# Performance work log

Measured on AMD Instinct MI355X. Metric: run time of the kernel, lower is better.

The kernel has to match this reference:

```python
import jax, jax.numpy as jnp
import numpy as np

T, B, C = 1024, 16, 1024
H, K, PAD_L = 16, 7, 3  # num_heads, kernel_size, padding_l
OUT = 1024


def setup_inputs() -> dict:
    key = jax.random.key(0)
    ks = jax.random.split(key, 8)
    s_in = 1.0 / np.sqrt(C)
    return {
        "x": jax.random.normal(ks[0], (T, B, C), dtype=jnp.float32),
        "W1": jax.random.normal(ks[1], (C, C), dtype=jnp.float32) * s_in,
        "b1": jnp.zeros((C,), dtype=jnp.float32),
        "Wq": jax.random.normal(ks[2], (C, H * K), dtype=jnp.float32) * s_in,
        "bq": jnp.zeros((H * K,), dtype=jnp.float32),
        "conv_bias": jax.random.normal(ks[3], (C,), dtype=jnp.float32) * 0.02,
        "W2": jax.random.normal(ks[4], (C, OUT), dtype=jnp.float32) * s_in,
        "b2": jnp.zeros((OUT,), dtype=jnp.float32),
    }


def reference(x, W1, b1, Wq, bq, conv_bias, W2, b2):
    # linear1 (glu=False -> no activation)
    h = x @ W1 + b1                       # [T, B, C]
    Tn, Bn, Cn = h.shape
    R = Cn // H                           # channels per head
    # dynamic filter prediction from query (= h), softmax over K taps
    w = (h @ Wq + bq).reshape(Tn, Bn, H, K)
    w = jax.nn.softmax(w, axis=-1)        # [T, B, H, K]
    # unfold1d: pad PAD_L left, K-1-PAD_L right along time, gather K-windows
    hp = jnp.pad(h, ((PAD_L, K - 1 - PAD_L), (0, 0), (0, 0)))
    win = jnp.stack([hp[k:k + Tn] for k in range(K)], axis=-1)  # [T, B, C, K]
    win = win.reshape(Tn, Bn, H, R, K)
    out = jnp.einsum('tbhrk,tbhk->tbhr', win, w).reshape(Tn, Bn, Cn)
    out = out + conv_bias                 # [T, B, C]
    return out @ W2 + b2                  # [T, B, OUT]
```

## Files before the change

kernel.cpp:

```cpp
#include <hip/hip_runtime.h>
#include <math.h>

#define T_DIM 1024
#define B_DIM 16
#define C_DIM 1024
#define H_DIM 16
#define K_TAPS 7
#define PAD_LEFT 3
#define OUT_DIM 1024
#define M_DIM (T_DIM * B_DIM)
#define HK 112
#define HKP 128
#define KD 1024
#define NT32 (KD / 32)

typedef __attribute__((ext_vector_type(8))) short bf16x8;
typedef __attribute__((ext_vector_type(4))) float f32x4;

__device__ __forceinline__ ushort f2bf(float f) {
    union { float f; unsigned u; } v; v.f = f;
    unsigned u = v.u;
    u += 0x7fffu + ((u >> 16) & 1u);
    return (ushort)(u >> 16);
}
__device__ __forceinline__ float bf2f(ushort h) {
    union { unsigned u; float f; } v; v.u = ((unsigned)h) << 16;
    return v.f;
}

__global__ __launch_bounds__(256) void cvt_bf16x8(const float* __restrict__ in,
                                                  ushort* __restrict__ out,
                                                  int n8) {
    int i = blockIdx.x * blockDim.x + threadIdx.x;
    if (i >= n8) return;
    const float4* p = (const float4*)in;
    float4 a = p[2 * i], b = p[2 * i + 1];
    uint4 o;
    o.x = (unsigned)f2bf(a.x) | ((unsigned)f2bf(a.y) << 16);
    o.y = (unsigned)f2bf(a.z) | ((unsigned)f2bf(a.w) << 16);
    o.z = (unsigned)f2bf(b.x) | ((unsigned)f2bf(b.y) << 16);
    o.w = (unsigned)f2bf(b.z) | ((unsigned)f2bf(b.w) << 16);
    ((uint4*)out)[i] = o;
}

__global__ void transpose_cvt(const float* __restrict__ W,
                              ushort* __restrict__ Wt,
                              int Kd, int N, int Npad) {
    __shared__ float tile[32][33];
    int n0 = blockIdx.x * 32, k0 = blockIdx.y * 32;
    int tx = threadIdx.x, ty = threadIdx.y;
#pragma unroll
    for (int j = 0; j < 4; ++j) {
        int k = k0 + ty * 4 + j;
        int n = n0 + tx;
        tile[ty * 4 + j][tx] = (n < N) ? W[(size_t)k * N + n] : 0.f;
    }
    __syncthreads();
#pragma unroll
    for (int j = 0; j < 4; ++j) {
        int n = n0 + ty * 4 + j;
        if (n < Npad)
            Wt[(size_t)n * Kd + k0 + tx] = f2bf(tile[tx][ty * 4 + j]);
    }
}

template <bool OUT_BF16>
__global__ __launch_bounds__(256, 2) void gemm_k32(
    const ushort* __restrict__ A, const ushort* __restrict__ Bt,
    const float* __restrict__ bias, void* __restrict__ Cp, int ldc) {
    __shared__ ushort Ab[2][256 * 32];
    __shared__ ushort Bb[2][128 * 32];

    const int tid  = threadIdx.x;
    const int lane = tid & 63;
    const int wid  = tid >> 6;
    const int wr = wid >> 1;
    const int wc = wid & 1;
    const int fr = lane & 15;
    const int fq = lane >> 4;

    const int orig = blockIdx.x;
    const int nid  = (orig & 7) * 64 + (orig >> 3);
    const int bm = (nid >> 3) * 256;
    const int bn = (nid & 7) * 128;

    const int rA   = tid >> 2;
    const int slA  = (tid & 3) * 8;
    const size_t srcA0 = (size_t)(bm + rA) * KD + slA;
    const size_t srcB0 = (size_t)(bn + rA) * KD + slA;

    const int aBase0 = (wr * 128 + fr) * 32 + fq * 8;
    const int bBase0 = (wc * 64 + fr) * 32 + fq * 8;

    f32x4 acc[8][4];
#pragma unroll
    for (int m = 0; m < 8; ++m)
#pragma unroll
        for (int n = 0; n < 4; ++n) acc[m][n] = (f32x4){0.f, 0.f, 0.f, 0.f};

    auto stage = [&](int buf, int t) {
        const ushort* Ap = A + srcA0 + t * 32;
        const ushort* Bp = Bt + srcB0 + t * 32;
#pragma unroll
        for (int i = 0; i < 4; ++i)
            __builtin_amdgcn_global_load_lds(
                (const __attribute__((address_space(1))) void*)(Ap + (size_t)i * 64 * KD),
                (__attribute__((address_space(3))) void*)(&Ab[buf][(i * 256 + wid * 64) * 8]),
                16, 0, 0);
#pragma unroll
        for (int i = 0; i < 2; ++i)
            __builtin_amdgcn_global_load_lds(
                (const __attribute__((address_space(1))) void*)(Bp + (size_t)i * 64 * KD),
                (__attribute__((address_space(3))) void*)(&Bb[buf][(i * 256 + wid * 64) * 8]),
                16, 0, 0);
    };

    stage(0, 0);
    stage(1, 1);
    asm volatile("s_waitcnt vmcnt(6)" ::: "memory");
    __builtin_amdgcn_sched_barrier(0);
    __builtin_amdgcn_s_barrier();

#pragma unroll 1
    for (int t = 0; t < NT32; ++t) {
        const int cur = t & 1;
        const ushort* Ac = &Ab[cur][0];
        const ushort* Bc = &Bb[cur][0];

        bf16x8 a[8], b[4];
#pragma unroll
        for (int n = 0; n < 4; ++n)
            b[n] = *(const bf16x8*)(Bc + bBase0 + n * 512);
#pragma unroll
        for (int m = 0; m < 8; ++m)
            a[m] = *(const bf16x8*)(Ac + aBase0 + m * 512);

        asm volatile("s_waitcnt lgkmcnt(0)" ::: "memory");
        __builtin_amdgcn_sched_barrier(0);
        __builtin_amdgcn_s_barrier();

        if (t < NT32 - 2) stage(cur, t + 2);

        __builtin_amdgcn_s_setprio(1);
#pragma unroll
        for (int m = 0; m < 8; ++m)
#pragma unroll
            for (int n = 0; n < 4; ++n)
                acc[m][n] = __builtin_amdgcn_mfma_f32_16x16x32_bf16(
                    a[m], b[n], acc[m][n], 0, 0, 0);
        __builtin_amdgcn_s_setprio(0);

        if (t < NT32 - 2) {
            asm volatile("s_waitcnt vmcnt(6)" ::: "memory");
        } else if (t == NT32 - 2) {
            asm volatile("s_waitcnt vmcnt(0)" ::: "memory");
        }
        __builtin_amdgcn_sched_barrier(0);
        if (t < NT32 - 1) __builtin_amdgcn_s_barrier();
    }

#pragma unroll
    for (int n = 0; n < 4; ++n) {
        int col = bn + wc * 64 + n * 16 + fr;
        float bv = bias[col];
#pragma unroll
        for (int m = 0; m < 8; ++m) {
#pragma unroll
            for (int r = 0; r < 4; ++r) {
                int row = bm + wr * 128 + m * 16 + fq * 4 + r;
                float v = acc[m][n][r] + bv;
                if (OUT_BF16)
                    ((ushort*)Cp)[(size_t)row * ldc + col] = f2bf(v);
                else
                    ((float*)Cp)[(size_t)row * ldc + col] = v;
            }
        }
    }
}

template <bool OUT_BF16, bool NGUARD>
__global__ __launch_bounds__(256) void gemm_mfma(const ushort* __restrict__ A,
                                                 const ushort* __restrict__ Bt,
                                                 const float* __restrict__ bias,
                                                 void* __restrict__ Cp,
                                                 int Kd, int N, int ldc) {
    __shared__ ushort Als[128 * 32];
    __shared__ ushort Bls[128 * 32];
    const int tid  = threadIdx.x;
    const int lane = tid & 63;
    const int wid  = tid >> 6;
    const int wr = wid >> 1, wc = wid & 1;
    const int bm = blockIdx.y * 128, bn = blockIdx.x * 128;
    const int fq = lane >> 4, fr = lane & 15;

    f32x4 acc[4][4];
#pragma unroll
    for (int m = 0; m < 4; ++m)
#pragma unroll
        for (int n = 0; n < 4; ++n) acc[m][n] = (f32x4){0.f, 0.f, 0.f, 0.f};

    const int c0 = wid * 128 + lane;
    const int c1 = c0 + 64;
    const int r0 = c0 >> 2, o0 = (c0 & 3) * 8;
    const int r1 = c1 >> 2, o1 = (c1 & 3) * 8;

    for (int k0 = 0; k0 < Kd; k0 += 32) {
        __builtin_amdgcn_global_load_lds(
            (const __attribute__((address_space(1))) void*)&A[(size_t)(bm + r0) * Kd + k0 + o0],
            (__attribute__((address_space(3))) void*)&Als[(wid * 2 + 0) * 512], 16, 0, 0);
        __builtin_amdgcn_global_load_lds(
            (const __attribute__((address_space(1))) void*)&A[(size_t)(bm + r1) * Kd + k0 + o1],
            (__attribute__((address_space(3))) void*)&Als[(wid * 2 + 1) * 512], 16, 0, 0);
        __builtin_amdgcn_global_load_lds(
            (const __attribute__((address_space(1))) void*)&Bt[(size_t)(bn + r0) * Kd + k0 + o0],
            (__attribute__((address_space(3))) void*)&Bls[(wid * 2 + 0) * 512], 16, 0, 0);
        __builtin_amdgcn_global_load_lds(
            (const __attribute__((address_space(1))) void*)&Bt[(size_t)(bn + r1) * Kd + k0 + o1],
            (__attribute__((address_space(3))) void*)&Bls[(wid * 2 + 1) * 512], 16, 0, 0);
        __syncthreads();

        bf16x8 af[4], bfr[4];
#pragma unroll
        for (int m = 0; m < 4; ++m)
            af[m] = *(const bf16x8*)&Als[(wr * 64 + m * 16 + fr) * 32 + fq * 8];
#pragma unroll
        for (int n = 0; n < 4; ++n)
            bfr[n] = *(const bf16x8*)&Bls[(wc * 64 + n * 16 + fr) * 32 + fq * 8];
#pragma unroll
        for (int m = 0; m < 4; ++m)
#pragma unroll
            for (int n = 0; n < 4; ++n)
                acc[m][n] = __builtin_amdgcn_mfma_f32_16x16x32_bf16(
                    af[m], bfr[n], acc[m][n], 0, 0, 0);
        __syncthreads();
    }

#pragma unroll
    for (int m = 0; m < 4; ++m) {
#pragma unroll
        for (int n = 0; n < 4; ++n) {
            int col = bn + wc * 64 + n * 16 + fr;
            if (NGUARD && col >= N) continue;
            float bv = bias[col];
#pragma unroll
            for (int r = 0; r < 4; ++r) {
                int row = bm + wr * 64 + m * 16 + fq * 4 + r;
                float v = acc[m][n][r] + bv;
                if (OUT_BF16)
                    ((ushort*)Cp)[(size_t)row * ldc + col] = f2bf(v);
                else
                    ((float*)Cp)[(size_t)row * ldc + col] = v;
            }
        }
    }
}

__global__ __launch_bounds__(256) void dynconv_bf16(const ushort* __restrict__ h,
                                                    const float* __restrict__ q,
                                                    const float* __restrict__ cbias,
                                                    ushort* __restrict__ out) {
    const int m = blockIdx.x;
    const int t = m >> 4;
    const int b = m & 15;

    __shared__ float wsm[HK];
    if (threadIdx.x < HK)
        wsm[threadIdx.x] = q[(size_t)m * HK + threadIdx.x];
    __syncthreads();
    if (threadIdx.x < H_DIM) {
        float* p = &wsm[threadIdx.x * K_TAPS];
        float mx = p[0];
#pragma unroll
        for (int k = 1; k < K_TAPS; ++k) mx = fmaxf(mx, p[k]);
        float e[K_TAPS], s = 0.f;
#pragma unroll
        for (int k = 0; k < K_TAPS; ++k) { e[k] = __expf(p[k] - mx); s += e[k]; }
        float inv = 1.f / s;
#pragma unroll
        for (int k = 0; k < K_TAPS; ++k) p[k] = e[k] * inv;
    }
    __syncthreads();

    const int c = threadIdx.x * 4;
    const int hh = c >> 6;

    float4 bias = *(const float4*)&cbias[c];
    float a0 = bias.x, a1 = bias.y, a2 = bias.z, a3 = bias.w;

#pragma unroll
    for (int k = 0; k < K_TAPS; ++k) {
        int tt = t + k - PAD_LEFT;
        if (tt < 0 || tt >= T_DIM) continue;
        ushort4 hv = *(const ushort4*)&h[((size_t)tt * B_DIM + b) * C_DIM + c];
        float wk = wsm[hh * K_TAPS + k];
        a0 = fmaf(bf2f(hv.x), wk, a0);
        a1 = fmaf(bf2f(hv.y), wk, a1);
        a2 = fmaf(bf2f(hv.z), wk, a2);
        a3 = fmaf(bf2f(hv.w), wk, a3);
    }
    ushort4 o;
    o.x = f2bf(a0); o.y = f2bf(a1); o.z = f2bf(a2); o.w = f2bf(a3);
    *(ushort4*)&out[(size_t)m * C_DIM + c] = o;
}

extern "C" void kernel_launch(void* const* d_in, const int* in_sizes, int n_in,
                              void* d_out, int out_size, void* d_ws,
                              size_t ws_size, hipStream_t stream) {
    const float* x     = (const float*)d_in[0];
    const float* W1    = (const float*)d_in[1];
    const float* b1    = (const float*)d_in[2];
    const float* Wq    = (const float*)d_in[3];
    const float* bq    = (const float*)d_in[4];
    const float* cbias = (const float*)d_in[5];
    const float* W2    = (const float*)d_in[6];
    const float* b2    = (const float*)d_in[7];
    float* out = (float*)d_out;

    ushort* xb    = (ushort*)d_ws;
    ushort* hb    = xb    + (size_t)M_DIM * C_DIM;
    ushort* convb = hb    + (size_t)M_DIM * C_DIM;
    ushort* W1t   = convb + (size_t)M_DIM * C_DIM;
    ushort* W2t   = W1t   + (size_t)C_DIM * C_DIM;
    ushort* Wqt   = W2t   + (size_t)C_DIM * OUT_DIM;
    float*  q     = (float*)(Wqt + (size_t)HKP * C_DIM);

    cvt_bf16x8<<<dim3(M_DIM * C_DIM / 8 / 256), dim3(256), 0, stream>>>(
        x, xb, M_DIM * C_DIM / 8);
    transpose_cvt<<<dim3(C_DIM / 32, C_DIM / 32), dim3(32, 8), 0, stream>>>(
        W1, W1t, C_DIM, C_DIM, C_DIM);
    transpose_cvt<<<dim3(HKP / 32, C_DIM / 32), dim3(32, 8), 0, stream>>>(
        Wq, Wqt, C_DIM, HK, HKP);
    transpose_cvt<<<dim3(OUT_DIM / 32, C_DIM / 32), dim3(32, 8), 0, stream>>>(
        W2, W2t, C_DIM, OUT_DIM, OUT_DIM);

    gemm_k32<true><<<dim3(512), dim3(256), 0, stream>>>(xb, W1t, b1, hb, C_DIM);

    gemm_mfma<false, true>
        <<<dim3(1, M_DIM / 128), dim3(256), 0, stream>>>(
            hb, Wqt, bq, q, C_DIM, HK, HK);

    dynconv_bf16<<<dim3(M_DIM), dim3(256), 0, stream>>>(hb, q, cbias, convb);

    gemm_k32<false><<<dim3(512), dim3(256), 0, stream>>>(convb, W2t, b2, out,
                                                         OUT_DIM);
}
```

Baseline: 171.7 us.

## Enlarge GEMM tiles to 256x256 with swizzled LDS and retile conv and small GEMM

The big GEMMs move from 256x128 tiles with K-step 32 to 256x256 tiles with K-step 64. They use an XOR-swizzled LDS layout and split each K-step into two MFMA halves, aiming to cut global and LDS traffic per flop and avoid bank conflicts. The three weight transposes are merged into one launch. The q-projection GEMM now uses 64-row tiles to get more blocks. The dynamic conv now stages a 22-row time window in LDS so each block handles 16 timesteps and reuses neighbouring rows. The cost is occupancy of one block per CU with 64 accumulator tiles and 128KB of LDS, and only 256 blocks for the big GEMMs.

```diff
diff --git a/kernel.cpp b/kernel.cpp
--- a/kernel.cpp
+++ b/kernel.cpp
@@ -12,7 +12,6 @@
 #define HK 112
 #define HKP 128
 #define KD 1024
-#define NT32 (KD / 32)
 
 typedef __attribute__((ext_vector_type(8))) short bf16x8;
 typedef __attribute__((ext_vector_type(4))) float f32x4;
@@ -43,11 +42,19 @@
     ((uint4*)out)[i] = o;
 }
 
-__global__ void transpose_cvt(const float* __restrict__ W,
-                              ushort* __restrict__ Wt,
-                              int Kd, int N, int Npad) {
+__global__ void transpose_all(const float* __restrict__ W1s,
+                              const float* __restrict__ Wqs,
+                              const float* __restrict__ W2s,
+                              ushort* __restrict__ W1t,
+                              ushort* __restrict__ Wqt,
+                              ushort* __restrict__ W2t) {
     __shared__ float tile[32][33];
-    int n0 = blockIdx.x * 32, k0 = blockIdx.y * 32;
+    int bx = blockIdx.x;
+    const float* W; ushort* Wt; int N, Npad, nb;
+    if (bx < 32)      { W = W1s; Wt = W1t; N = 1024; Npad = 1024; nb = bx; }
+    else if (bx < 36) { W = Wqs; Wt = Wqt; N = 112;  Npad = 128;  nb = bx - 32; }
+    else              { W = W2s; Wt = W2t; N = 1024; Npad = 1024; nb = bx - 36; }
+    int n0 = nb * 32, k0 = blockIdx.y * 32;
     int tx = threadIdx.x, ty = threadIdx.y;
 #pragma unroll
     for (int j = 0; j < 4; ++j) {
@@ -60,16 +67,16 @@
     for (int j = 0; j < 4; ++j) {
         int n = n0 + ty * 4 + j;
         if (n < Npad)
-            Wt[(size_t)n * Kd + k0 + tx] = f2bf(tile[tx][ty * 4 + j]);
+            Wt[(size_t)n * KD + k0 + tx] = f2bf(tile[tx][ty * 4 + j]);
     }
 }
 
 template <bool OUT_BF16>
-__global__ __launch_bounds__(256, 2) void gemm_k32(
+__global__ __launch_bounds__(256, 1) void gemm_big(
     const ushort* __restrict__ A, const ushort* __restrict__ Bt,
     const float* __restrict__ bias, void* __restrict__ Cp, int ldc) {
-    __shared__ ushort Ab[2][256 * 32];
-    __shared__ ushort Bb[2][128 * 32];
+    __shared__ ushort Ab[2][256 * 64];
+    __shared__ ushort Bb[2][256 * 64];
 
     const int tid  = threadIdx.x;
     const int lane = tid & 63;
@@ -80,88 +87,109 @@
     const int fq = lane >> 4;
 
     const int orig = blockIdx.x;
-    const int nid  = (orig & 7) * 64 + (orig >> 3);
-    const int bm = (nid >> 3) * 256;
-    const int bn = (nid & 7) * 128;
-
-    const int rA   = tid >> 2;
-    const int slA  = (tid & 3) * 8;
-    const size_t srcA0 = (size_t)(bm + rA) * KD + slA;
-    const size_t srcB0 = (size_t)(bn + rA) * KD + slA;
-
-    const int aBase0 = (wr * 128 + fr) * 32 + fq * 8;
-    const int bBase0 = (wc * 64 + fr) * 32 + fq * 8;
-
-    f32x4 acc[8][4];
+    const int nid  = (orig & 7) * 32 + (orig >> 3);
+    const int bm = (nid >> 2) * 256;
+    const int bn = (nid & 3) * 256;
+
+    const int srow = tid >> 3;
+    const int scol = ((tid & 7) ^ ((tid >> 3) & 7)) * 8;
+    const size_t srcA0 = (size_t)(bm + srow) * KD + scol;
+    const size_t srcB0 = (size_t)(bn + srow) * KD + scol;
+
+    const int swb = (fq ^ (fr & 3)) * 8 + ((fr >> 2) & 1) * 32;
+    const int aOff0 = (wr * 128 + fr) * 64 + swb;
+    const int bOff0 = (wc * 128 + fr) * 64 + swb;
+    const int aOff1 = aOff0 ^ 32;
+    const int bOff1 = bOff0 ^ 32;
+
+    f32x4 acc[8][8];
 #pragma unroll
     for (int m = 0; m < 8; ++m)
 #pragma unroll
-        for (int n = 0; n < 4; ++n) acc[m][n] = (f32x4){0.f, 0.f, 0.f, 0.f};
+        for (int n = 0; n < 8; ++n) acc[m][n] = (f32x4){0.f, 0.f, 0.f, 0.f};
 
     auto stage = [&](int buf, int t) {
-        const ushort* Ap = A + srcA0 + t * 32;
-        const ushort* Bp = Bt + srcB0 + t * 32;
-#pragma unroll
-        for (int i = 0; i < 4; ++i)
+        const ushort* Ap = A + srcA0 + t * 64;
+        const ushort* Bp = Bt + srcB0 + t * 64;
+#pragma unroll
+        for (int i = 0; i < 8; ++i)
             __builtin_amdgcn_global_load_lds(
-                (const __attribute__((address_space(1))) void*)(Ap + (size_t)i * 64 * KD),
+                (const __attribute__((address_space(1))) void*)(Ap + (size_t)i * 32 * KD),
                 (__attribute__((address_space(3))) void*)(&Ab[buf][(i * 256 + wid * 64) * 8]),
                 16, 0, 0);
 #pragma unroll
-        for (int i = 0; i < 2; ++i)
+        for (int i = 0; i < 8; ++i)
             __builtin_amdgcn_global_load_lds(
-                (const __attribute__((address_space(1))) void*)(Bp + (size_t)i * 64 * KD),
+                (const __attribute__((address_space(1))) void*)(Bp + (size_t)i * 32 * KD),
                 (__attribute__((address_space(3))) void*)(&Bb[buf][(i * 256 + wid * 64) * 8]),
                 16, 0, 0);
     };
 
     stage(0, 0);
     stage(1, 1);
-    asm volatile("s_waitcnt vmcnt(6)" ::: "memory");
+    asm volatile("s_waitcnt vmcnt(16)" ::: "memory");
     __builtin_amdgcn_sched_barrier(0);
     __builtin_amdgcn_s_barrier();
 
 #pragma unroll 1
-    for (int t = 0; t < NT32; ++t) {
+    for (int t = 0; t < 16; ++t) {
         const int cur = t & 1;
         const ushort* Ac = &Ab[cur][0];
         const ushort* Bc = &Bb[cur][0];
 
-        bf16x8 a[8], b[4];
-#pragma unroll
-        for (int n = 0; n < 4; ++n)
-            b[n] = *(const bf16x8*)(Bc + bBase0 + n * 512);
+        {
+            bf16x8 a0[8], b0[8];
+#pragma unroll
+            for (int n = 0; n < 8; ++n)
+                b0[n] = *(const bf16x8*)(Bc + bOff0 + n * 1024);
+#pragma unroll
+            for (int m = 0; m < 8; ++m)
+                a0[m] = *(const bf16x8*)(Ac + aOff0 + m * 1024);
+            __builtin_amdgcn_s_setprio(1);
+#pragma unroll
+            for (int m = 0; m < 8; ++m)
+#pragma unroll
+                for (int n = 0; n < 8; ++n)
+                    acc[m][n] = __builtin_amdgcn_mfma_f32_16x16x32_bf16(
+                        a0[m], b0[n], acc[m][n], 0, 0, 0);
+            __builtin_amdgcn_s_setprio(0);
+        }
+
+        bf16x8 a1[8], b1[8];
+#pragma unroll
+        for (int n = 0; n < 8; ++n)
+            b1[n] = *(const bf16x8*)(Bc + bOff1 + n * 1024);
 #pragma unroll
         for (int m = 0; m < 8; ++m)
-            a[m] = *(const bf16x8*)(Ac + aBase0 + m * 512);
+            a1[m] = *(const bf16x8*)(Ac + aOff1 + m * 1024);
 
         asm volatile("s_waitcnt lgkmcnt(0)" ::: "memory");
         __builtin_amdgcn_sched_barrier(0);
         __builtin_amdgcn_s_barrier();
 
-        if (t < NT32 - 2) stage(cur, t + 2);
+        if (t < 14) stage(cur, t + 2);
 
         __builtin_amdgcn_s_setprio(1);
 #pragma unroll
         for (int m = 0; m < 8; ++m)
 #pragma unroll
-            for (int n = 0; n < 4; ++n)
+            for (int n = 0; n < 8; ++n)
                 acc[m][n] = __builtin_amdgcn_mfma_f32_16x16x32_bf16(
-                    a[m], b[n], acc[m][n], 0, 0, 0);
+                    a1[m], b1[n], acc[m][n], 0, 0, 0);
         __builtin_amdgcn_s_setprio(0);
 
-        if (t < NT32 - 2) {
-            asm volatile("s_waitcnt vmcnt(6)" ::: "memory");
-        } else if (t == NT32 - 2) {
+        if (t < 14) {
+            asm volatile("s_waitcnt vmcnt(16)" ::: "memory");
+        } else if (t == 14) {
             asm volatile("s_waitcnt vmcnt(0)" ::: "memory");
         }
         __builtin_amdgcn_sched_barrier(0);
-        if (t < NT32 - 1) __builtin_amdgcn_s_barrier();
-    }
-
-#pragma unroll
-    for (int n = 0; n < 4; ++n) {
-        int col = bn + wc * 64 + n * 16 + fr;
+        if (t < 15) __builtin_amdgcn_s_barrier();
+    }
+
+#pragma unroll
+    for (int n = 0; n < 8; ++n) {
+        int col = bn + wc * 128 + n * 16 + fr;
         float bv = bias[col];
 #pragma unroll
         for (int m = 0; m < 8; ++m) {
@@ -178,56 +206,48 @@
     }
 }
 
-template <bool OUT_BF16, bool NGUARD>
-__global__ __launch_bounds__(256) void gemm_mfma(const ushort* __restrict__ A,
-                                                 const ushort* __restrict__ Bt,
-                                                 const float* __restrict__ bias,
-                                                 void* __restrict__ Cp,
-                                                 int Kd, int N, int ldc) {
-    __shared__ ushort Als[128 * 32];
+__global__ __launch_bounds__(256) void gemm_small(const ushort* __restrict__ A,
+                                                  const ushort* __restrict__ Bt,
+                                                  const float* __restrict__ bias,
+                                                  float* __restrict__ Cp) {
+    __shared__ ushort Als[64 * 32];
     __shared__ ushort Bls[128 * 32];
     const int tid  = threadIdx.x;
     const int lane = tid & 63;
     const int wid  = tid >> 6;
     const int wr = wid >> 1, wc = wid & 1;
-    const int bm = blockIdx.y * 128, bn = blockIdx.x * 128;
+    const int bm = blockIdx.y * 64;
     const int fq = lane >> 4, fr = lane & 15;
 
-    f32x4 acc[4][4];
-#pragma unroll
-    for (int m = 0; m < 4; ++m)
+    f32x4 acc[2][4];
+#pragma unroll
+    for (int m = 0; m < 2; ++m)
 #pragma unroll
         for (int n = 0; n < 4; ++n) acc[m][n] = (f32x4){0.f, 0.f, 0.f, 0.f};
 
-    const int c0 = wid * 128 + lane;
-    const int c1 = c0 + 64;
-    const int r0 = c0 >> 2, o0 = (c0 & 3) * 8;
-    const int r1 = c1 >> 2, o1 = (c1 & 3) * 8;
-
-    for (int k0 = 0; k0 < Kd; k0 += 32) {
+    const int rA = tid >> 2, oA = (tid & 3) * 8;
+    for (int k0 = 0; k0 < KD; k0 += 32) {
         __builtin_amdgcn_global_load_lds(
-            (const __attribute__((address_space(1))) void*)&A[(size_t)(bm + r0) * Kd + k0 + o0],
-            (__attribute__((address_space(3))) void*)&Als[(wid * 2 + 0) * 512], 16, 0, 0);
-        __builtin_amdgcn_global_load_lds(
-            (const __attribute__((address_space(1))) void*)&A[(size_t)(bm + r1) * Kd + k0 + o1],
-            (__attribute__((address_space(3))) void*)&Als[(wid * 2 + 1) * 512], 16, 0, 0);
-        __builtin_amdgcn_global_load_lds(
-            (const __attribute__((address_space(1))) void*)&Bt[(size_t)(bn + r0) * Kd + k0 + o0],
-            (__attribute__((address_space(3))) void*)&Bls[(wid * 2 + 0) * 512], 16, 0, 0);
-        __builtin_amdgcn_global_load_lds(
-            (const __attribute__((address_space(1))) void*)&Bt[(size_t)(bn + r1) * Kd + k0 + o1],
-            (__attribute__((address_space(3))) void*)&Bls[(wid * 2 + 1) * 512], 16, 0, 0);
+            (const __attribute__((address_space(1))) void*)&A[(size_t)(bm + rA) * KD + k0 + oA],
+            (__attribute__((address_space(3))) void*)&Als[wid * 64 * 8], 16, 0, 0);
+#pragma unroll
+        for (int i = 0; i < 2; ++i) {
+            int c = i * 256 + tid;
+            __builtin_amdgcn_global_load_lds(
+                (const __attribute__((address_space(1))) void*)&Bt[(size_t)(c >> 2) * KD + k0 + (c & 3) * 8],
+                (__attribute__((address_space(3))) void*)&Bls[(i * 256 + wid * 64) * 8], 16, 0, 0);
+        }
         __syncthreads();
 
-        bf16x8 af[4], bfr[4];
-#pragma unroll
-        for (int m = 0; m < 4; ++m)
-            af[m] = *(const bf16x8*)&Als[(wr * 64 + m * 16 + fr) * 32 + fq * 8];
+        bf16x8 af[2], bfr[4];
+#pragma unroll
+        for (int m = 0; m < 2; ++m)
+            af[m] = *(const bf16x8*)&Als[(wr * 32 + m * 16 + fr) * 32 + fq * 8];
 #pragma unroll
         for (int n = 0; n < 4; ++n)
             bfr[n] = *(const bf16x8*)&Bls[(wc * 64 + n * 16 + fr) * 32 + fq * 8];
 #pragma unroll
-        for (int m = 0; m < 4; ++m)
+        for (int m = 0; m < 2; ++m)
 #pragma unroll
             for (int n = 0; n < 4; ++n)
                 acc[m][n] = __builtin_amdgcn_mfma_f32_16x16x32_bf16(
@@ -236,39 +256,44 @@
     }
 
 #pragma unroll
-    for (int m = 0; m < 4; ++m) {
+    for (int m = 0; m < 2; ++m) {
 #pragma unroll
         for (int n = 0; n < 4; ++n) {
-            int col = bn + wc * 64 + n * 16 + fr;
-            if (NGUARD && col >= N) continue;
+            int col = wc * 64 + n * 16 + fr;
+            if (col >= HK) continue;
             float bv = bias[col];
 #pragma unroll
             for (int r = 0; r < 4; ++r) {
-                int row = bm + wr * 64 + m * 16 + fq * 4 + r;
-                float v = acc[m][n][r] + bv;
-                if (OUT_BF16)
-                    ((ushort*)Cp)[(size_t)row * ldc + col] = f2bf(v);
-                else
-                    ((float*)Cp)[(size_t)row * ldc + col] = v;
+                int row = bm + wr * 32 + m * 16 + fq * 4 + r;
+                Cp[(size_t)row * HK + col] = acc[m][n][r] + bv;
             }
         }
     }
 }
 
-__global__ __launch_bounds__(256) void dynconv_bf16(const ushort* __restrict__ h,
-                                                    const float* __restrict__ q,
-                                                    const float* __restrict__ cbias,
-                                                    ushort* __restrict__ out) {
-    const int m = blockIdx.x;
-    const int t = m >> 4;
-    const int b = m & 15;
-
-    __shared__ float wsm[HK];
-    if (threadIdx.x < HK)
-        wsm[threadIdx.x] = q[(size_t)m * HK + threadIdx.x];
-    __syncthreads();
-    if (threadIdx.x < H_DIM) {
-        float* p = &wsm[threadIdx.x * K_TAPS];
+__global__ __launch_bounds__(256) void dynconv2(const ushort* __restrict__ h,
+                                                const float* __restrict__ q,
+                                                const float* __restrict__ cbias,
+                                                ushort* __restrict__ out) {
+    __shared__ ushort hw[22][1024];
+    __shared__ float wsm[16][HK];
+    const int tid = threadIdx.x;
+    const int b  = blockIdx.x & 15;
+    const int t0 = (blockIdx.x >> 4) << 4;
+
+    for (int i = tid; i < 22 * 128; i += 256) {
+        int wrow = i >> 7;
+        int c8   = (i & 127) * 8;
+        int tt   = t0 + wrow - PAD_LEFT;
+        uint4 v = make_uint4(0, 0, 0, 0);
+        if (tt >= 0 && tt < T_DIM)
+            v = *(const uint4*)&h[((size_t)tt * B_DIM + b) * C_DIM + c8];
+        *(uint4*)&hw[wrow][c8] = v;
+    }
+    {
+        int tl = tid >> 4, hh = tid & 15;
+        int m = (t0 + tl) * B_DIM + b;
+        const float* p = &q[(size_t)m * HK + hh * K_TAPS];
         float mx = p[0];
 #pragma unroll
         for (int k = 1; k < K_TAPS; ++k) mx = fmaxf(mx, p[k]);
@@ -277,30 +302,29 @@
         for (int k = 0; k < K_TAPS; ++k) { e[k] = __expf(p[k] - mx); s += e[k]; }
         float inv = 1.f / s;
 #pragma unroll
-        for (int k = 0; k < K_TAPS; ++k) p[k] = e[k] * inv;
+        for (int k = 0; k < K_TAPS; ++k) wsm[tl][hh * K_TAPS + k] = e[k] * inv;
     }
     __syncthreads();
 
-    const int c = threadIdx.x * 4;
+    const int c  = tid * 4;
     const int hh = c >> 6;
-
     float4 bias = *(const float4*)&cbias[c];
-    float a0 = bias.x, a1 = bias.y, a2 = bias.z, a3 = bias.w;
-
-#pragma unroll
-    for (int k = 0; k < K_TAPS; ++k) {
-        int tt = t + k - PAD_LEFT;
-        if (tt < 0 || tt >= T_DIM) continue;
-        ushort4 hv = *(const ushort4*)&h[((size_t)tt * B_DIM + b) * C_DIM + c];
-        float wk = wsm[hh * K_TAPS + k];
-        a0 = fmaf(bf2f(hv.x), wk, a0);
-        a1 = fmaf(bf2f(hv.y), wk, a1);
-        a2 = fmaf(bf2f(hv.z), wk, a2);
-        a3 = fmaf(bf2f(hv.w), wk, a3);
-    }
-    ushort4 o;
-    o.x = f2bf(a0); o.y = f2bf(a1); o.z = f2bf(a2); o.w = f2bf(a3);
-    *(ushort4*)&out[(size_t)m * C_DIM + c] = o;
+
+    for (int tl = 0; tl < 16; ++tl) {
+        float a0 = bias.x, a1 = bias.y, a2 = bias.z, a3 = bias.w;
+#pragma unroll
+        for (int k = 0; k < K_TAPS; ++k) {
+            ushort4 hv = *(const ushort4*)&hw[tl + k][c];
+            float wk = wsm[tl][hh * K_TAPS + k];
+            a0 = fmaf(bf2f(hv.x), wk, a0);
+            a1 = fmaf(bf2f(hv.y), wk, a1);
+            a2 = fmaf(bf2f(hv.z), wk, a2);
+            a3 = fmaf(bf2f(hv.w), wk, a3);
+        }
+        ushort4 o;
+        o.x = f2bf(a0); o.y = f2bf(a1); o.z = f2bf(a2); o.w = f2bf(a3);
+        *(ushort4*)&out[((size_t)(t0 + tl) * B_DIM + b) * C_DIM + c] = o;
+    }
 }
 
 extern "C" void kernel_launch(void* const* d_in, const int* in_sizes, int n_in,
@@ -326,21 +350,16 @@
 
     cvt_bf16x8<<<dim3(M_DIM * C_DIM / 8 / 256), dim3(256), 0, stream>>>(
         x, xb, M_DIM * C_DIM / 8);
-    transpose_cvt<<<dim3(C_DIM / 32, C_DIM / 32), dim3(32, 8), 0, stream>>>(
-        W1, W1t, C_DIM, C_DIM, C_DIM);
-    transpose_cvt<<<dim3(HKP / 32, C_DIM / 32), dim3(32, 8), 0, stream>>>(
-        Wq, Wqt, C_DIM, HK, HKP);
-    transpose_cvt<<<dim3(OUT_DIM / 32, C_DIM / 32), dim3(32, 8), 0, stream>>>(
-        W2, W2t, C_DIM, OUT_DIM, OUT_DIM);
-
-    gemm_k32<true><<<dim3(512), dim3(256), 0, stream>>>(xb, W1t, b1, hb, C_DIM);
-
-    gemm_mfma<false, true>
-        <<<dim3(1, M_DIM / 128), dim3(256), 0, stream>>>(
-            hb, Wqt, bq, q, C_DIM, HK, HK);
-
-    dynconv_bf16<<<dim3(M_DIM), dim3(256), 0, stream>>>(hb, q, cbias, convb);
-
-    gemm_k32<false><<<dim3(512), dim3(256), 0, stream>>>(convb, W2t, b2, out,
+    transpose_all<<<dim3(68, 32), dim3(32, 8), 0, stream>>>(
+        W1, Wq, W2, W1t, Wqt, W2t);
+
+    gemm_big<true><<<dim3(256), dim3(256), 0, stream>>>(xb, W1t, b1, hb, C_DIM);
+
+    gemm_small<<<dim3(1, M_DIM / 64), dim3(256), 0, stream>>>(hb, Wqt, bq, q);
+
+    dynconv2<<<dim3(B_DIM * T_DIM / 16), dim3(256), 0, stream>>>(
+        hb, q, cbias, convb);
+
+    gemm_big<false><<<dim3(256), dim3(256), 0, stream>>>(convb, W2t, b2, out,
                                                          OUT_DIM);
 }
```

New measurement: 200.7 us. 16.9% more time.
